# Kernel tuning notes

Measured on AMD Instinct MI355X. Metric: run time of the kernel, lower is better.

Reference implementation:

```python
import jax, jax.numpy as jnp
import numpy as np
from jax.scipy.special import logsumexp

B, T, S, V = 64, 1024, 512, 1024


def setup_inputs() -> dict:
    key = jax.random.key(0)
    k_obs, k_emis, k_trans, k_prior = jax.random.split(key, 4)
    observations = jax.random.randint(k_obs, (B, T), 0, V, dtype=jnp.int32)
    emission_table = jax.random.normal(k_emis, (V, S), dtype=jnp.float32)
    transitions = jax.random.normal(k_trans, (S, S), dtype=jnp.float32)
    prior = jax.random.normal(k_prior, (S,), dtype=jnp.float32)
    return {
        "observations": observations,
        "emission_table": emission_table,
        "transitions": transitions,
        "prior": prior,
    }


def reference(observations, emission_table, transitions, prior):
    # alpha_0[b, s] = emission_logits(obs_0)[b, s] + prior[s]
    alpha0 = emission_table[observations[:, 0]] + prior  # [B, S]

    def step(alpha, obs_t):
        # new_alpha[b, j] = emis[b, j] + logsumexp_i(alpha[b, i] + trans[i, j])
        e = emission_table[obs_t]  # [B, S]
        a = e + logsumexp(alpha[:, :, None] + transitions[None, :, :], axis=1)
        return a, None

    # scan over time steps 1..T-1; xs is [T-1, B]
    alpha, _ = jax.lax.scan(step, alpha0, observations[:, 1:].T)
    return logsumexp(alpha, axis=1)  # [B]
```

## Files before the change

### kernel.cpp

```cpp
#include <hip/hip_runtime.h>


constexpr int Bn = 64, Tn = 1024, Sn = 512;
#define L2E 1.44269504f

typedef int v4i __attribute__((ext_vector_type(4)));

#if __has_builtin(__builtin_amdgcn_update_dpp)
template <int CTRL>
__device__ __forceinline__ float dpp_fmax(float x) {
    int s = __builtin_bit_cast(int, x);
    int d = __builtin_amdgcn_update_dpp(s, s, CTRL, 0xf, 0xf, false);
    return fmaxf(x, __builtin_bit_cast(float, d));
}
__device__ __forceinline__ float wave_max64(float x) {
    x = dpp_fmax<0x121>(x);
    x = dpp_fmax<0x122>(x);
    x = dpp_fmax<0x124>(x);
    x = dpp_fmax<0x128>(x);
    x = dpp_fmax<0x142>(x);
    x = dpp_fmax<0x143>(x);
    return __builtin_bit_cast(float,
        __builtin_amdgcn_readlane(__builtin_bit_cast(int, x), 63));
}
#else
__device__ __forceinline__ float wave_max64(float x) {
    #pragma unroll
    for (int off = 32; off; off >>= 1) x = fmaxf(x, __shfl_xor(x, off, 64));
    return x;
}
#endif

__device__ __forceinline__ int bfrag_addr(int i, int c) {
    return ((((c >> 4) * 8 + (i >> 6)) * 64) + ((i >> 4) & 3) * 16 + (c & 15)) * 16
           + (i & 15);
}

__global__ __launch_bounds__(256) void prep_rows(
    const float* __restrict__ trans, unsigned char* __restrict__ EqB,
    float* __restrict__ rowmax)
{
    const int i = blockIdx.x;
    const int j = threadIdx.x;
    const int lane = j & 63, wv = j >> 6;
    float t0 = trans[i * Sn + j];
    float t1 = trans[i * Sn + j + 256];
    float m = fmaxf(t0, t1);
    #pragma unroll
    for (int off = 32; off; off >>= 1) m = fmaxf(m, __shfl_xor(m, off, 64));
    __shared__ float rm[4];
    if (lane == 0) rm[wv] = m;
    __syncthreads();
    m = fmaxf(fmaxf(rm[0], rm[1]), fmaxf(rm[2], rm[3]));
    if (j == 0) rowmax[i] = m;
    int q0 = __float2int_rn(127.f * __expf(t0 - m));
    int q1 = __float2int_rn(127.f * __expf(t1 - m));
    EqB[bfrag_addr(i, j)] = (unsigned char)q0;
    EqB[bfrag_addr(i, j + 256)] = (unsigned char)q1;
}

__global__ __launch_bounds__(512) void prep_scale(
    const float* __restrict__ rowmax, float* __restrict__ lr,
    float* __restrict__ Cp)
{
    const int i = threadIdx.x;
    const int lane = i & 63, wv = i >> 6;
    float m = rowmax[i];
    float rm = m;
    #pragma unroll
    for (int off = 32; off; off >>= 1) rm = fmaxf(rm, __shfl_xor(rm, off, 64));
    __shared__ float red[8];
    if (lane == 0) red[wv] = rm;
    __syncthreads();
    float RM = red[0];
    #pragma unroll
    for (int w = 1; w < 8; ++w) RM = fmaxf(RM, red[w]);
    lr[i] = (m - RM) * L2E + 6.98868469f;
    if (i == 0) *Cp = RM - 9.68837417f;
}

__global__ __launch_bounds__(512, 2) void hmm_fwd(
    const int* __restrict__ obs,
    const float* __restrict__ emis,
    const float* __restrict__ prior,
    const v4i* __restrict__ EqB4,
    const float* __restrict__ lr,
    const float* __restrict__ Cp,
    float* __restrict__ out)
{
    const int b = blockIdx.x;
    const int tid = threadIdx.x;
    const int lane = tid & 63, wv = tid >> 6;
    const int q = lane >> 4;

    __shared__ int obs_s[Tn + 1];
    __shared__ __align__(16) unsigned char Pq[2][Sn];
    __shared__ __align__(16) float redm[2][8];
    __shared__ float reds[8];

    int o0 = obs[b * Tn + tid];
    int o1 = obs[b * Tn + 512 + tid];
    obs_s[tid] = o0;
    obs_s[tid + 512] = o1;
    if (tid == 511) obs_s[Tn] = o1;

    v4i Bf[4][8];
    #pragma unroll
    for (int tau = 0; tau < 4; ++tau)
        #pragma unroll
        for (int kap = 0; kap < 8; ++kap)
            Bf[tau][kap] = EqB4[((wv * 4 + tau) * 8 + kap) * 64 + lane];

    const float lr_t = lr[tid];
    const float C = *Cp;

    __syncthreads();

    float a = emis[obs_s[0] * Sn + tid] + prior[tid];
    float e_next = emis[obs_s[1] * Sn + tid];

    for (int t = 1; t < Tn; ++t) {
        const int pb = t & 1;

        float mw = wave_max64(a);
        if (lane == 0) redm[pb][wv] = mw;
        __syncthreads();
        float4 r0 = *(const float4*)&redm[pb][0];
        float4 r1 = *(const float4*)&redm[pb][4];
        float m = fmaxf(fmaxf(fmaxf(r0.x, r0.y), fmaxf(r0.z, r0.w)),
                        fmaxf(fmaxf(r1.x, r1.y), fmaxf(r1.z, r1.w)));

        int gi = __float2int_rn(exp2f(fmaf(a - m, L2E, lr_t)));
        Pq[pb][tid] = (unsigned char)gi;
        __syncthreads();

        float e_cur = e_next;
        e_next = emis[obs_s[t + 1] * Sn + tid];

        const unsigned char* Pbase = Pq[pb] + q * 16;
        v4i Af[8];
        #pragma unroll
        for (int kap = 0; kap < 8; ++kap)
            Af[kap] = *(const v4i*)(Pbase + kap * 64);

        v4i acc[4];
        #pragma unroll
        for (int tau = 0; tau < 4; ++tau) {
            v4i z = {0, 0, 0, 0};
            #pragma unroll
            for (int kap = 0; kap < 8; ++kap)
                z = __builtin_amdgcn_mfma_i32_16x16x64_i8(Af[kap], Bf[tau][kap],
                                                          z, 0, 0, 0);
            acc[tau] = z;
        }

        int idot = (lane < 16) ? acc[0].x
                 : (lane < 32) ? acc[1].x
                 : (lane < 48) ? acc[2].x
                               : acc[3].x;

        a = e_cur + m + C + __logf((float)idot);
    }

    float m = a;
    #pragma unroll
    for (int off = 32; off; off >>= 1) m = fmaxf(m, __shfl_xor(m, off, 64));
    if (lane == 0) redm[0][wv] = m;
    __syncthreads();
    #pragma unroll
    for (int w = 0; w < 8; ++w) m = fmaxf(m, redm[0][w]);

    float s = __expf(a - m);
    #pragma unroll
    for (int off = 32; off; off >>= 1) s += __shfl_xor(s, off, 64);
    if (lane == 0) reds[wv] = s;
    __syncthreads();
    if (tid == 0) {
        float tot = 0.f;
        #pragma unroll
        for (int w = 0; w < 8; ++w) tot += reds[w];
        out[b] = m + __logf(tot);
    }
}

extern "C" void kernel_launch(void* const* d_in, const int* in_sizes, int n_in,
                              void* d_out, int out_size, void* d_ws, size_t ws_size,
                              hipStream_t stream) {
    const int*   obs   = (const int*)d_in[0];
    const float* emis  = (const float*)d_in[1];
    const float* trans = (const float*)d_in[2];
    const float* prior = (const float*)d_in[3];
    float* out = (float*)d_out;

    unsigned char* EqB = (unsigned char*)d_ws;
    float* rowmax = (float*)(EqB + Sn * Sn);
    float* lr     = rowmax + Sn;
    float* Cp     = lr + Sn;

    prep_rows<<<Sn, 256, 0, stream>>>(trans, EqB, rowmax);
    prep_scale<<<1, Sn, 0, stream>>>(rowmax, lr, Cp);
    hmm_fwd<<<Bn, Sn, 0, stream>>>(obs, emis, prior,
                                   (const v4i*)EqB, lr, Cp, out);
}
```

Measured before the change: 987.1 us.

## Interleave two batch sequences per block and track forward variables in linear space

Each block now processes two batch elements with staggered phases, so one sequence's MFMA dot product and max reduction overlap the other's quantization step. Each time step keeps one barrier per sequence instead of two barriers per sequence. The recurrence moves from log space to scaled linear space with an accumulated log normalizer, swapping exp/log work for reciprocals and multiplies. Only 32 blocks are launched, so half as many CUs are busy. Longer per-block serial work is traded for latency hiding.

```diff
diff --git a/kernel.cpp b/kernel.cpp
--- a/kernel.cpp
+++ b/kernel.cpp
@@ -30,6 +30,38 @@
     return x;
 }
 #endif
+
+__device__ __forceinline__ float tree8(const float* p) {
+    float4 r0 = *(const float4*)p;
+    float4 r1 = *(const float4*)(p + 4);
+    return fmaxf(fmaxf(fmaxf(r0.x, r0.y), fmaxf(r0.z, r0.w)),
+                 fmaxf(fmaxf(r1.x, r1.y), fmaxf(r1.z, r1.w)));
+}
+
+__device__ __forceinline__ float mfma_dot(const unsigned char* Pq_,
+                                          const v4i (&Bf)[4][8],
+                                          int q, int lane) {
+    const unsigned char* Pb = Pq_ + q * 16;
+    v4i Af[8];
+    #pragma unroll
+    for (int kap = 0; kap < 8; ++kap)
+        Af[kap] = *(const v4i*)(Pb + kap * 64);
+    v4i acc[4];
+    #pragma unroll
+    for (int tau = 0; tau < 4; ++tau) {
+        v4i z = {0, 0, 0, 0};
+        #pragma unroll
+        for (int kap = 0; kap < 8; ++kap)
+            z = __builtin_amdgcn_mfma_i32_16x16x64_i8(Af[kap], Bf[tau][kap],
+                                                      z, 0, 0, 0);
+        acc[tau] = z;
+    }
+    int idot = (lane < 16) ? acc[0].x
+             : (lane < 32) ? acc[1].x
+             : (lane < 48) ? acc[2].x
+                           : acc[3].x;
+    return (float)idot;
+}
 
 __device__ __forceinline__ int bfrag_addr(int i, int c) {
     return ((((c >> 4) * 8 + (i >> 6)) * 64) + ((i >> 4) & 3) * 16 + (c & 15)) * 16
@@ -79,7 +111,7 @@
     if (i == 0) *Cp = RM - 9.68837417f;
 }
 
-__global__ __launch_bounds__(512, 2) void hmm_fwd(
+__global__ __launch_bounds__(512, 2) void hmm_fwd2(
     const int* __restrict__ obs,
     const float* __restrict__ emis,
     const float* __restrict__ prior,
@@ -88,21 +120,21 @@
     const float* __restrict__ Cp,
     float* __restrict__ out)
 {
-    const int b = blockIdx.x;
+    const int bA = blockIdx.x * 2, bB = bA + 1;
     const int tid = threadIdx.x;
     const int lane = tid & 63, wv = tid >> 6;
     const int q = lane >> 4;
 
-    __shared__ int obs_s[Tn + 1];
-    __shared__ __align__(16) unsigned char Pq[2][Sn];
-    __shared__ __align__(16) float redm[2][8];
-    __shared__ float reds[8];
-
-    int o0 = obs[b * Tn + tid];
-    int o1 = obs[b * Tn + 512 + tid];
-    obs_s[tid] = o0;
-    obs_s[tid + 512] = o1;
-    if (tid == 511) obs_s[Tn] = o1;
+    __shared__ int obsA_s[Tn + 1], obsB_s[Tn + 1];
+    __shared__ __align__(16) unsigned char PqA[Sn], PqB[Sn];
+    __shared__ __align__(16) float redmA[8], redmB[8];
+    __shared__ float reds[16];
+
+    int a0 = obs[bA * Tn + tid], a1 = obs[bA * Tn + 512 + tid];
+    int b0 = obs[bB * Tn + tid], b1 = obs[bB * Tn + 512 + tid];
+    obsA_s[tid] = a0; obsA_s[tid + 512] = a1;
+    obsB_s[tid] = b0; obsB_s[tid + 512] = b1;
+    if (tid == 511) { obsA_s[Tn] = a1; obsB_s[Tn] = b1; }
 
     v4i Bf[4][8];
     #pragma unroll
@@ -111,75 +143,89 @@
         for (int kap = 0; kap < 8; ++kap)
             Bf[tau][kap] = EqB4[((wv * 4 + tau) * 8 + kap) * 64 + lane];
 
-    const float lr_t = lr[tid];
+    const float lrf = exp2f(lr[tid]);
     const float C = *Cp;
 
     __syncthreads();
 
-    float a = emis[obs_s[0] * Sn + tid] + prior[tid];
-    float e_next = emis[obs_s[1] * Sn + tid];
+    float wdA = __expf(emis[obsA_s[0] * Sn + tid] + prior[tid]);
+    float wdB = __expf(emis[obsB_s[0] * Sn + tid] + prior[tid]);
+    float lwA = lrf * wdA, lwB = lrf * wdB;
+    float SA = 0.f, SB = 0.f;
+    float eNA = emis[obsA_s[1] * Sn + tid];
+    float eNB = emis[obsB_s[1] * Sn + tid];
+
+    float mwB = wave_max64(wdB);
+    if (lane == 0) redmB[wv] = mwB;
+    __syncthreads();
+    {
+        float WB = tree8(redmB);
+        int giB = __float2int_rn(lwB * __builtin_amdgcn_rcpf(WB));
+        PqB[tid] = (unsigned char)giB;
+        SB += __logf(WB) + C;
+    }
+    float mwA = wave_max64(wdA);
+    if (lane == 0) redmA[wv] = mwA;
 
     for (int t = 1; t < Tn; ++t) {
-        const int pb = t & 1;
-
-        float mw = wave_max64(a);
-        if (lane == 0) redm[pb][wv] = mw;
         __syncthreads();
-        float4 r0 = *(const float4*)&redm[pb][0];
-        float4 r1 = *(const float4*)&redm[pb][4];
-        float m = fmaxf(fmaxf(fmaxf(r0.x, r0.y), fmaxf(r0.z, r0.w)),
-                        fmaxf(fmaxf(r1.x, r1.y), fmaxf(r1.z, r1.w)));
-
-        int gi = __float2int_rn(exp2f(fmaf(a - m, L2E, lr_t)));
-        Pq[pb][tid] = (unsigned char)gi;
+        float weCA = __expf(eNA);
+        float weCB = __expf(eNB);
+
+        {
+            float WA = tree8(redmA);
+            int giA = __float2int_rn(lwA * __builtin_amdgcn_rcpf(WA));
+            PqA[tid] = (unsigned char)giA;
+            SA += __logf(WA) + C;
+        }
+        eNA = emis[obsA_s[t + 1] * Sn + tid];
+
+        float dfB = mfma_dot(PqB, Bf, q, lane);
+        wdB = weCB * dfB;
+        lwB = lrf * wdB;
+        float mB = wave_max64(wdB);
+        if (lane == 0) redmB[wv] = mB;
+
         __syncthreads();
-
-        float e_cur = e_next;
-        e_next = emis[obs_s[t + 1] * Sn + tid];
-
-        const unsigned char* Pbase = Pq[pb] + q * 16;
-        v4i Af[8];
-        #pragma unroll
-        for (int kap = 0; kap < 8; ++kap)
-            Af[kap] = *(const v4i*)(Pbase + kap * 64);
-
-        v4i acc[4];
-        #pragma unroll
-        for (int tau = 0; tau < 4; ++tau) {
-            v4i z = {0, 0, 0, 0};
-            #pragma unroll
-            for (int kap = 0; kap < 8; ++kap)
-                z = __builtin_amdgcn_mfma_i32_16x16x64_i8(Af[kap], Bf[tau][kap],
-                                                          z, 0, 0, 0);
-            acc[tau] = z;
+        eNB = emis[obsB_s[t + 1] * Sn + tid];
+
+        if (t < Tn - 1) {
+            float WB = tree8(redmB);
+            int giB = __float2int_rn(lwB * __builtin_amdgcn_rcpf(WB));
+            PqB[tid] = (unsigned char)giB;
+            SB += __logf(WB) + C;
         }
 
-        int idot = (lane < 16) ? acc[0].x
-                 : (lane < 32) ? acc[1].x
-                 : (lane < 48) ? acc[2].x
-                               : acc[3].x;
-
-        a = e_cur + m + C + __logf((float)idot);
-    }
-
-    float m = a;
-    #pragma unroll
-    for (int off = 32; off; off >>= 1) m = fmaxf(m, __shfl_xor(m, off, 64));
-    if (lane == 0) redm[0][wv] = m;
-    __syncthreads();
-    #pragma unroll
-    for (int w = 0; w < 8; ++w) m = fmaxf(m, redm[0][w]);
-
-    float s = __expf(a - m);
-    #pragma unroll
-    for (int off = 32; off; off >>= 1) s += __shfl_xor(s, off, 64);
-    if (lane == 0) reds[wv] = s;
+        float dfA = mfma_dot(PqA, Bf, q, lane);
+        wdA = weCA * dfA;
+        lwA = lrf * wdA;
+        float mA = wave_max64(wdA);
+        if (lane == 0) redmA[wv] = mA;
+    }
+
+    __syncthreads();
+    float WfA = tree8(redmA);
+    float WfB = tree8(redmB);
+    float sA = wdA * __builtin_amdgcn_rcpf(WfA);
+    float sB = wdB * __builtin_amdgcn_rcpf(WfB);
+    #pragma unroll
+    for (int off = 32; off; off >>= 1) {
+        sA += __shfl_xor(sA, off, 64);
+        sB += __shfl_xor(sB, off, 64);
+    }
+    if (lane == 0) { reds[wv] = sA; reds[8 + wv] = sB; }
     __syncthreads();
     if (tid == 0) {
         float tot = 0.f;
         #pragma unroll
         for (int w = 0; w < 8; ++w) tot += reds[w];
-        out[b] = m + __logf(tot);
+        out[bA] = SA + __logf(WfA) + __logf(tot);
+    }
+    if (tid == 64) {
+        float tot = 0.f;
+        #pragma unroll
+        for (int w = 0; w < 8; ++w) tot += reds[8 + w];
+        out[bB] = SB + __logf(WfB) + __logf(tot);
     }
 }
 
@@ -199,6 +245,6 @@
 
     prep_rows<<<Sn, 256, 0, stream>>>(trans, EqB, rowmax);
     prep_scale<<<1, Sn, 0, stream>>>(rowmax, lr, Cp);
-    hmm_fwd<<<Bn, Sn, 0, stream>>>(obs, emis, prior,
-                                   (const v4i*)EqB, lr, Cp, out);
-}
+    hmm_fwd2<<<Bn / 2, Sn, 0, stream>>>(obs, emis, prior,
+                                        (const v4i*)EqB, lr, Cp, out);
+}
```

Measured after the change: 1.588 ms. +60.9%, slower.
